# Optimization experiments

Measured on AMD Instinct MI355X. Metric: run time of the kernel, lower is better.

Reference implementation:

```python
import jax, jax.numpy as jnp
import numpy as np

B, T, E, H = 256, 128, 300, 2048


def setup_inputs() -> dict:
    key = jax.random.key(0)
    k0, k1, k2, k3, k4 = jax.random.split(key, 5)
    s = 1.0 / np.sqrt(H)  # PyTorch LSTM init range
    return {
        "x": jax.random.normal(k0, (B, T, E), dtype=jnp.float32),
        "W_ih": jax.random.uniform(k1, (4 * H, E), dtype=jnp.float32, minval=-s, maxval=s),
        "W_hh": jax.random.uniform(k2, (4 * H, H), dtype=jnp.float32, minval=-s, maxval=s),
        "b_ih": jax.random.uniform(k3, (4 * H,), dtype=jnp.float32, minval=-s, maxval=s),
        "b_hh": jax.random.uniform(k4, (4 * H,), dtype=jnp.float32, minval=-s, maxval=s),
    }


def reference(x, W_ih, W_hh, b_ih, b_hh):
    # x: [B, T, E]; returns final hidden state h_T: [B, H]
    Bn = x.shape[0]
    Hn = W_hh.shape[1]
    # Precompute input-to-gate projection for all timesteps: [B, T, 4H]
    x_gates = jnp.einsum('bte,ge->btg', x, W_ih) + b_ih + b_hh

    def step(carry, xg_t):
        h, c = carry
        gates = xg_t + h @ W_hh.T  # [B, 4H]
        i, f, g, o = jnp.split(gates, 4, axis=-1)  # PyTorch gate order i,f,g,o
        i = jax.nn.sigmoid(i)
        f = jax.nn.sigmoid(f)
        g = jnp.tanh(g)
        o = jax.nn.sigmoid(o)
        c = f * c + i * g
        h = o * jnp.tanh(c)
        return (h, c), None

    h0 = jnp.zeros((Bn, Hn), dtype=x.dtype)
    c0 = jnp.zeros((Bn, Hn), dtype=x.dtype)
    (h_T, _), _ = jax.lax.scan(step, (h0, c0), jnp.swapaxes(x_gates, 0, 1))
    return h_T
```

## Files before the change

### kernel.cpp

```cpp
#include <hip/hip_runtime.h>

typedef unsigned short u16;
typedef unsigned int u32;
typedef __bf16 bf16x8 __attribute__((ext_vector_type(8)));
typedef float f32x4 __attribute__((ext_vector_type(4)));

#define B_ 256
#define T_ 128
#define E_ 300
#define EP 320
#define H_ 2048
#define G_ 8192

#define OFF_XBF   0UL
#define OFF_WIH   20971520UL
#define OFF_WHH   26214400UL
#define OFF_BIAS  59768832UL
#define OFF_HBUF  59801600UL
#define OFF_BAR   61898752UL

#define GLDS16(gp, sp)                                                    \
  __builtin_amdgcn_global_load_lds(                                       \
      (__attribute__((address_space(1))) void*)(void*)(gp),               \
      (__attribute__((address_space(3))) void*)(sp), 16, 0, 0)
#define GLDS16C(gp, sp)                                                   \
  __builtin_amdgcn_global_load_lds(                                       \
      (__attribute__((address_space(1))) void*)(void*)(gp),               \
      (__attribute__((address_space(3))) void*)(sp), 16, 0, 17)

__device__ __forceinline__ u16 f2bf(float f) {
  u32 u = __builtin_bit_cast(u32, f);
  return (u16)((u + 0x7FFFu + ((u >> 16) & 1u)) >> 16);
}
__device__ __forceinline__ float sigm_f(float x) {
  return __builtin_amdgcn_rcpf(1.0f + __expf(-x));
}
__device__ __forceinline__ float tanh_f(float x) {
  return 1.0f - 2.0f * __builtin_amdgcn_rcpf(1.0f + __expf(2.0f * x));
}

__global__ void prep_kernel(const float* __restrict__ x, const float* __restrict__ Wih,
                            const float* __restrict__ Whh, const float* __restrict__ bih,
                            const float* __restrict__ bhh, u16* __restrict__ xbf,
                            u16* __restrict__ wihb, u16* __restrict__ whhb,
                            float* __restrict__ biasc, u32* __restrict__ bar) {
  const long NX = (long)T_ * B_ * EP;
  const long NWIH = (long)G_ * EP;
  const long NWHH = (long)G_ * H_;
  const long NBS = G_;
  const long NBAR = T_;
  const long total = NX + NWIH + NWHH + NBS + NBAR;
  for (long q = (long)blockIdx.x * blockDim.x + threadIdx.x; q < total;
       q += (long)gridDim.x * blockDim.x) {
    long r = q;
    if (r < NX) {
      int t = (int)(r / (B_ * EP));
      int rem = (int)(r % (B_ * EP));
      int b = rem / EP, e = rem % EP;
      float v = (e < E_) ? x[((long)b * T_ + t) * E_ + e] : 0.0f;
      xbf[r] = f2bf(v);
    } else if ((r -= NX) < NWIH) {
      int n = (int)(r / EP), e = (int)(r % EP);
      wihb[r] = f2bf((e < E_) ? Wih[(long)n * E_ + e] : 0.0f);
    } else if ((r -= NWIH) < NWHH) {
      whhb[r] = f2bf(Whh[r]);
    } else if ((r -= NWHH) < NBS) {
      biasc[r] = bih[r] + bhh[r];
    } else {
      r -= NBS;
      bar[r] = 0;
    }
  }
}

__global__ void __launch_bounds__(256, 1)
lstm_kernel(const u16* __restrict__ xbf, const u16* __restrict__ wihb,
            const u16* __restrict__ whhb, const float* __restrict__ biasc,
            u16* __restrict__ hbuf, u32* __restrict__ bar, float* __restrict__ out) {
  __shared__ __align__(16) u16 As[2][64 * 64];
  __shared__ __align__(16) u16 Bs[2][128 * 64];

  const int tid = threadIdx.x;
  const int l = tid & 63;
  const int w = tid >> 6;
  const int wr = w >> 1, wj = w & 1;
  const int bid = blockIdx.x;
  const int b0 = (bid >> 6) << 6;
  const int j0 = (bid & 63) << 5;
  const int jc = j0 + (wj << 4) + (l & 15);
  const int cgl = (tid & 7) ^ ((tid >> 3) & 7);

  const float bi = biasc[jc];
  const float bff = biasc[2048 + jc];
  const float bg = biasc[4096 + jc];
  const float bo = biasc[6144 + jc];

  float cst[2][4];
#pragma unroll
  for (int mi = 0; mi < 2; ++mi)
#pragma unroll
    for (int r = 0; r < 4; ++r) cst[mi][r] = 0.0f;

  auto stageA = [&](const u16* srcA, int strA, int kk, int p, bool coh) {
    u16* Ad = &As[p][w * 512];
#pragma unroll
    for (int i = 0; i < 2; ++i) {
      int slot = i * 256 + tid;
      const u16* g = srcA + (size_t)(slot >> 3) * strA + kk + cgl * 8;
      if (coh) { GLDS16C(g, Ad + i * 2048); } else { GLDS16(g, Ad + i * 2048); }
    }
  };
  auto stageB = [&](const u16* srcB, int strB, int kk, int p) {
    u16* Bd = &Bs[p][w * 512];
#pragma unroll
    for (int i = 0; i < 4; ++i) {
      int slot = i * 256 + tid;
      int nl = slot >> 3;
      int grow = ((nl >> 5) << 11) + j0 + (nl & 31);
      const u16* g = srcB + (size_t)grow * strB + kk + cgl * 8;
      GLDS16(g, Bd + i * 2048);
    }
  };

#pragma unroll 1
  for (int t = 0; t < T_; ++t) {
    const u16* hcur = hbuf + (size_t)(t & 1) * (B_ * H_) + (size_t)b0 * H_;
    u16* hnxt = hbuf + (size_t)((t + 1) & 1) * (B_ * H_);
    const u16* xsrc = xbf + (size_t)t * (B_ * EP) + (size_t)b0 * EP;

    f32x4 acc[2][4];
#pragma unroll
    for (int mi = 0; mi < 2; ++mi)
#pragma unroll
      for (int g = 0; g < 4; ++g) acc[mi][g] = (f32x4){0.f, 0.f, 0.f, 0.f};

    auto compute = [&](int p) {
#pragma unroll
      for (int k2 = 0; k2 < 2; ++k2) {
        int cp = ((k2 << 2) + (l >> 4)) ^ (l & 7);
        const u16* ap = &As[p][((wr << 5) + (l & 15)) * 64 + cp * 8];
        bf16x8 a0 = *(const bf16x8*)ap;
        bf16x8 a1 = *(const bf16x8*)(ap + 1024);
        const u16* bp = &Bs[p][((wj << 4) + (l & 15)) * 64 + cp * 8];
        bf16x8 bv0 = *(const bf16x8*)bp;
        bf16x8 bv1 = *(const bf16x8*)(bp + 2048);
        bf16x8 bv2 = *(const bf16x8*)(bp + 4096);
        bf16x8 bv3 = *(const bf16x8*)(bp + 6144);
        acc[0][0] = __builtin_amdgcn_mfma_f32_16x16x32_bf16(a0, bv0, acc[0][0], 0, 0, 0);
        acc[0][1] = __builtin_amdgcn_mfma_f32_16x16x32_bf16(a0, bv1, acc[0][1], 0, 0, 0);
        acc[0][2] = __builtin_amdgcn_mfma_f32_16x16x32_bf16(a0, bv2, acc[0][2], 0, 0, 0);
        acc[0][3] = __builtin_amdgcn_mfma_f32_16x16x32_bf16(a0, bv3, acc[0][3], 0, 0, 0);
        acc[1][0] = __builtin_amdgcn_mfma_f32_16x16x32_bf16(a1, bv0, acc[1][0], 0, 0, 0);
        acc[1][1] = __builtin_amdgcn_mfma_f32_16x16x32_bf16(a1, bv1, acc[1][1], 0, 0, 0);
        acc[1][2] = __builtin_amdgcn_mfma_f32_16x16x32_bf16(a1, bv2, acc[1][2], 0, 0, 0);
        acc[1][3] = __builtin_amdgcn_mfma_f32_16x16x32_bf16(a1, bv3, acc[1][3], 0, 0, 0);
      }
    };

    int p = 0;
    stageA(xsrc, EP, 0, 0, false);
    stageB(wihb, EP, 0, 0);
    __syncthreads();
#pragma unroll 1
    for (int kx = 0; kx < 5; ++kx) {
      if (kx < 4) {
        stageA(xsrc, EP, (kx + 1) << 6, p ^ 1, false);
        stageB(wihb, EP, (kx + 1) << 6, p ^ 1);
      }
      compute(p);
      __syncthreads();
      p ^= 1;
    }

    if (t > 0) {
      if (tid == 0) {
        while (__hip_atomic_load(&bar[t - 1], __ATOMIC_RELAXED,
                                 __HIP_MEMORY_SCOPE_AGENT) < 256u)
          __builtin_amdgcn_s_sleep(2);
      }
      __syncthreads();
      stageA(hcur, H_, 0, p, true);
      stageB(whhb, H_, 0, p);
      __syncthreads();
#pragma unroll 1
      for (int kh = 0; kh < 32; ++kh) {
        if (kh < 31) {
          stageA(hcur, H_, (kh + 1) << 6, p ^ 1, true);
          stageB(whhb, H_, (kh + 1) << 6, p ^ 1);
        }
        compute(p);
        __syncthreads();
        p ^= 1;
      }
    }

#pragma unroll
    for (int mi = 0; mi < 2; ++mi) {
#pragma unroll
      for (int r = 0; r < 4; ++r) {
        float ig = sigm_f(acc[mi][0][r] + bi);
        float fg = sigm_f(acc[mi][1][r] + bff);
        float gg = tanh_f(acc[mi][2][r] + bg);
        float og = sigm_f(acc[mi][3][r] + bo);
        float c = fg * cst[mi][r] + ig * gg;
        cst[mi][r] = c;
        float h = og * tanh_f(c);
        int row = b0 + (wr << 5) + (mi << 4) + ((l >> 4) << 2) + r;
        if (t < T_ - 1) {
          u16 hv = f2bf(h);
          u16* hp = hnxt + (size_t)row * H_ + jc;
          asm volatile("global_store_short %0, %1, off sc0 sc1"
                       :: "v"(hp), "v"((u32)hv) : "memory");
        } else {
          out[(size_t)row * H_ + jc] = h;
        }
      }
    }

    if (t < T_ - 1) {
      __builtin_amdgcn_s_waitcnt(0);
      __syncthreads();
      if (tid == 0)
        __hip_atomic_fetch_add(&bar[t], 1u, __ATOMIC_RELAXED,
                               __HIP_MEMORY_SCOPE_AGENT);
    }
  }
}

extern "C" void kernel_launch(void* const* d_in, const int* in_sizes, int n_in,
                              void* d_out, int out_size, void* d_ws, size_t ws_size,
                              hipStream_t stream) {
  const float* x = (const float*)d_in[0];
  const float* Wih = (const float*)d_in[1];
  const float* Whh = (const float*)d_in[2];
  const float* bih = (const float*)d_in[3];
  const float* bhh = (const float*)d_in[4];
  char* ws = (char*)d_ws;
  u16* xbf = (u16*)(ws + OFF_XBF);
  u16* wihb = (u16*)(ws + OFF_WIH);
  u16* whhb = (u16*)(ws + OFF_WHH);
  float* biasc = (float*)(ws + OFF_BIAS);
  u16* hbuf = (u16*)(ws + OFF_HBUF);
  u32* bar = (u32*)(ws + OFF_BAR);
  float* out = (float*)d_out;

  hipLaunchKernelGGL(prep_kernel, dim3(2048), dim3(256), 0, stream,
                     x, Wih, Whh, bih, bhh, xbf, wihb, whhb, biasc, bar);

  void* args[] = {(void*)&xbf, (void*)&wihb, (void*)&whhb,
                  (void*)&biasc, (void*)&hbuf, (void*)&bar, (void*)&out};
  hipLaunchCooperativeKernel((void*)lstm_kernel, dim3(256), dim3(256), args, 0, stream);
}
```

Baseline: 3.783 ms.

## Load GEMM operands directly into registers and give each timestep its own h buffer

Drops the LDS staging (global_load_lds with a swizzle, plus __syncthreads per k-step) and has each wave load its A and B fragments straight from global memory into registers, double-buffered in registers. The ping-pong h buffer becomes a per-timestep buffer, and the flag value read from the barrier (always below 2^31, so it adds 0) is folded into the h address so the compiler cannot hoist or cache the h loads ahead of the spin. This removes LDS round-trips and block-wide barriers, but each wave now issues redundant, less coalesced global loads for shared tiles. The h loads also lose the coherent cache-bypass flag.

After: 7.268 ms. 1.92x slower.

```diff
diff --git a/kernel.cpp b/kernel.cpp
--- a/kernel.cpp
+++ b/kernel.cpp
@@ -16,17 +16,8 @@
 #define OFF_WIH   20971520UL
 #define OFF_WHH   26214400UL
 #define OFF_BIAS  59768832UL
-#define OFF_HBUF  59801600UL
-#define OFF_BAR   61898752UL
-
-#define GLDS16(gp, sp)                                                    \
-  __builtin_amdgcn_global_load_lds(                                       \
-      (__attribute__((address_space(1))) void*)(void*)(gp),               \
-      (__attribute__((address_space(3))) void*)(sp), 16, 0, 0)
-#define GLDS16C(gp, sp)                                                   \
-  __builtin_amdgcn_global_load_lds(                                       \
-      (__attribute__((address_space(1))) void*)(void*)(gp),               \
-      (__attribute__((address_space(3))) void*)(sp), 16, 0, 17)
+#define OFF_BAR   59801600UL
+#define OFF_HBUF  59802112UL
 
 __device__ __forceinline__ u16 f2bf(float f) {
   u32 u = __builtin_bit_cast(u32, f);
@@ -76,10 +67,7 @@
 __global__ void __launch_bounds__(256, 1)
 lstm_kernel(const u16* __restrict__ xbf, const u16* __restrict__ wihb,
             const u16* __restrict__ whhb, const float* __restrict__ biasc,
-            u16* __restrict__ hbuf, u32* __restrict__ bar, float* __restrict__ out) {
-  __shared__ __align__(16) u16 As[2][64 * 64];
-  __shared__ __align__(16) u16 Bs[2][128 * 64];
-
+            u16* __restrict__ hbufs, u32* __restrict__ bar, float* __restrict__ out) {
   const int tid = threadIdx.x;
   const int l = tid & 63;
   const int w = tid >> 6;
@@ -87,8 +75,9 @@
   const int bid = blockIdx.x;
   const int b0 = (bid >> 6) << 6;
   const int j0 = (bid & 63) << 5;
+  const int arow = (wr << 5) + (l & 15);
+  const int koff = (l >> 4) << 3;
   const int jc = j0 + (wj << 4) + (l & 15);
-  const int cgl = (tid & 7) ^ ((tid >> 3) & 7);
 
   const float bi = biasc[jc];
   const float bff = biasc[2048 + jc];
@@ -101,99 +90,70 @@
 #pragma unroll
     for (int r = 0; r < 4; ++r) cst[mi][r] = 0.0f;
 
-  auto stageA = [&](const u16* srcA, int strA, int kk, int p, bool coh) {
-    u16* Ad = &As[p][w * 512];
-#pragma unroll
-    for (int i = 0; i < 2; ++i) {
-      int slot = i * 256 + tid;
-      const u16* g = srcA + (size_t)(slot >> 3) * strA + kk + cgl * 8;
-      if (coh) { GLDS16C(g, Ad + i * 2048); } else { GLDS16(g, Ad + i * 2048); }
-    }
-  };
-  auto stageB = [&](const u16* srcB, int strB, int kk, int p) {
-    u16* Bd = &Bs[p][w * 512];
-#pragma unroll
-    for (int i = 0; i < 4; ++i) {
-      int slot = i * 256 + tid;
-      int nl = slot >> 3;
-      int grow = ((nl >> 5) << 11) + j0 + (nl & 31);
-      const u16* g = srcB + (size_t)grow * strB + kk + cgl * 8;
-      GLDS16(g, Bd + i * 2048);
+  __shared__ u32 fv_sh;
+
+  f32x4 acc[2][4];
+
+  auto gemm_phase = [&](const u16* asrc, int astr, const u16* bsrc, int bstr,
+                        int kiters) {
+    bf16x8 af[2][2][2];
+    bf16x8 bfr[2][2][4];
+    auto ld = [&](int buf, int kk) {
+#pragma unroll
+      for (int mi = 0; mi < 2; ++mi)
+#pragma unroll
+        for (int k2 = 0; k2 < 2; ++k2)
+          af[buf][mi][k2] = *(const bf16x8*)(asrc +
+              (size_t)(arow + (mi << 4)) * astr + kk + (k2 << 5) + koff);
+#pragma unroll
+      for (int k2 = 0; k2 < 2; ++k2)
+#pragma unroll
+        for (int g = 0; g < 4; ++g)
+          bfr[buf][k2][g] = *(const bf16x8*)(bsrc +
+              (size_t)((g << 11) + jc) * bstr + kk + (k2 << 5) + koff);
+    };
+    ld(0, 0);
+#pragma unroll 2
+    for (int k = 0; k < kiters; ++k) {
+      int cur = k & 1;
+      if (k + 1 < kiters) ld(cur ^ 1, (k + 1) << 6);
+#pragma unroll
+      for (int k2 = 0; k2 < 2; ++k2)
+#pragma unroll
+        for (int g = 0; g < 4; ++g) {
+          acc[0][g] = __builtin_amdgcn_mfma_f32_16x16x32_bf16(
+              af[cur][0][k2], bfr[cur][k2][g], acc[0][g], 0, 0, 0);
+          acc[1][g] = __builtin_amdgcn_mfma_f32_16x16x32_bf16(
+              af[cur][1][k2], bfr[cur][k2][g], acc[1][g], 0, 0, 0);
+        }
     }
   };
 
 #pragma unroll 1
   for (int t = 0; t < T_; ++t) {
-    const u16* hcur = hbuf + (size_t)(t & 1) * (B_ * H_) + (size_t)b0 * H_;
-    u16* hnxt = hbuf + (size_t)((t + 1) & 1) * (B_ * H_);
+#pragma unroll
+    for (int mi = 0; mi < 2; ++mi)
+#pragma unroll
+      for (int g = 0; g < 4; ++g) acc[mi][g] = (f32x4){0.f, 0.f, 0.f, 0.f};
+
     const u16* xsrc = xbf + (size_t)t * (B_ * EP) + (size_t)b0 * EP;
-
-    f32x4 acc[2][4];
-#pragma unroll
-    for (int mi = 0; mi < 2; ++mi)
-#pragma unroll
-      for (int g = 0; g < 4; ++g) acc[mi][g] = (f32x4){0.f, 0.f, 0.f, 0.f};
-
-    auto compute = [&](int p) {
-#pragma unroll
-      for (int k2 = 0; k2 < 2; ++k2) {
-        int cp = ((k2 << 2) + (l >> 4)) ^ (l & 7);
-        const u16* ap = &As[p][((wr << 5) + (l & 15)) * 64 + cp * 8];
-        bf16x8 a0 = *(const bf16x8*)ap;
-        bf16x8 a1 = *(const bf16x8*)(ap + 1024);
-        const u16* bp = &Bs[p][((wj << 4) + (l & 15)) * 64 + cp * 8];
-        bf16x8 bv0 = *(const bf16x8*)bp;
-        bf16x8 bv1 = *(const bf16x8*)(bp + 2048);
-        bf16x8 bv2 = *(const bf16x8*)(bp + 4096);
-        bf16x8 bv3 = *(const bf16x8*)(bp + 6144);
-        acc[0][0] = __builtin_amdgcn_mfma_f32_16x16x32_bf16(a0, bv0, acc[0][0], 0, 0, 0);
-        acc[0][1] = __builtin_amdgcn_mfma_f32_16x16x32_bf16(a0, bv1, acc[0][1], 0, 0, 0);
-        acc[0][2] = __builtin_amdgcn_mfma_f32_16x16x32_bf16(a0, bv2, acc[0][2], 0, 0, 0);
-        acc[0][3] = __builtin_amdgcn_mfma_f32_16x16x32_bf16(a0, bv3, acc[0][3], 0, 0, 0);
-        acc[1][0] = __builtin_amdgcn_mfma_f32_16x16x32_bf16(a1, bv0, acc[1][0], 0, 0, 0);
-        acc[1][1] = __builtin_amdgcn_mfma_f32_16x16x32_bf16(a1, bv1, acc[1][1], 0, 0, 0);
-        acc[1][2] = __builtin_amdgcn_mfma_f32_16x16x32_bf16(a1, bv2, acc[1][2], 0, 0, 0);
-        acc[1][3] = __builtin_amdgcn_mfma_f32_16x16x32_bf16(a1, bv3, acc[1][3], 0, 0, 0);
-      }
-    };
-
-    int p = 0;
-    stageA(xsrc, EP, 0, 0, false);
-    stageB(wihb, EP, 0, 0);
-    __syncthreads();
-#pragma unroll 1
-    for (int kx = 0; kx < 5; ++kx) {
-      if (kx < 4) {
-        stageA(xsrc, EP, (kx + 1) << 6, p ^ 1, false);
-        stageB(wihb, EP, (kx + 1) << 6, p ^ 1);
-      }
-      compute(p);
-      __syncthreads();
-      p ^= 1;
-    }
+    gemm_phase(xsrc, EP, wihb, EP, 5);
 
     if (t > 0) {
       if (tid == 0) {
-        while (__hip_atomic_load(&bar[t - 1], __ATOMIC_RELAXED,
-                                 __HIP_MEMORY_SCOPE_AGENT) < 256u)
+        u32 f;
+        while ((f = __hip_atomic_load(&bar[t - 1], __ATOMIC_RELAXED,
+                                      __HIP_MEMORY_SCOPE_AGENT)) < 256u)
           __builtin_amdgcn_s_sleep(2);
+        fv_sh = f;
       }
       __syncthreads();
-      stageA(hcur, H_, 0, p, true);
-      stageB(whhb, H_, 0, p);
-      __syncthreads();
-#pragma unroll 1
-      for (int kh = 0; kh < 32; ++kh) {
-        if (kh < 31) {
-          stageA(hcur, H_, (kh + 1) << 6, p ^ 1, true);
-          stageB(whhb, H_, (kh + 1) << 6, p ^ 1);
-        }
-        compute(p);
-        __syncthreads();
-        p ^= 1;
-      }
-    }
-
+      const u16* hsrc = hbufs + (size_t)(t - 1) * (B_ * H_) +
+                        (size_t)b0 * H_ + (fv_sh >> 31);
+      gemm_phase(hsrc, H_, whhb, H_, 32);
+    }
+
+    u16* hnxt = hbufs + (size_t)t * (B_ * H_);
 #pragma unroll
     for (int mi = 0; mi < 2; ++mi) {
 #pragma unroll
@@ -240,14 +200,14 @@
   u16* wihb = (u16*)(ws + OFF_WIH);
   u16* whhb = (u16*)(ws + OFF_WHH);
   float* biasc = (float*)(ws + OFF_BIAS);
-  u16* hbuf = (u16*)(ws + OFF_HBUF);
   u32* bar = (u32*)(ws + OFF_BAR);
+  u16* hbufs = (u16*)(ws + OFF_HBUF);
   float* out = (float*)d_out;
 
   hipLaunchKernelGGL(prep_kernel, dim3(2048), dim3(256), 0, stream,
                      x, Wih, Whh, bih, bhh, xbf, wihb, whhb, biasc, bar);
 
   void* args[] = {(void*)&xbf, (void*)&wihb, (void*)&whhb,
-                  (void*)&biasc, (void*)&hbuf, (void*)&bar, (void*)&out};
+                  (void*)&biasc, (void*)&hbufs, (void*)&bar, (void*)&out};
   hipLaunchCooperativeKernel((void*)lstm_kernel, dim3(256), dim3(256), args, 0, stream);
 }
```

## Store each step's hidden state in its own buffer and drop coherent loads

Applied to the files above, without the earlier changes.

Each timestep now writes h to its own slice of a T-deep buffer instead of ping-ponging between two, so reads of h no longer need the sc0/sc1 coherent cache policy and use a nontemporal hint instead. Since no buffer is ever reused, stale cache lines cannot alias across steps. The flag value read from the barrier is folded into the address (always zero) to create a dependency. The cooperative launch is replaced by a normal launch. This trades a much larger workspace and reliance on fresh addresses for cheaper cached loads, and drops the co-residency guarantee for the spin barrier.

Result: slower. 4.853 ms (+28.3%).

```diff
diff --git a/kernel.cpp b/kernel.cpp
--- a/kernel.cpp
+++ b/kernel.cpp
@@ -16,17 +16,17 @@
 #define OFF_WIH   20971520UL
 #define OFF_WHH   26214400UL
 #define OFF_BIAS  59768832UL
-#define OFF_HBUF  59801600UL
-#define OFF_BAR   61898752UL
+#define OFF_BAR   59801600UL
+#define OFF_HBUF  59802112UL
 
 #define GLDS16(gp, sp)                                                    \
   __builtin_amdgcn_global_load_lds(                                       \
       (__attribute__((address_space(1))) void*)(void*)(gp),               \
       (__attribute__((address_space(3))) void*)(sp), 16, 0, 0)
-#define GLDS16C(gp, sp)                                                   \
+#define GLDS16NT(gp, sp)                                                  \
   __builtin_amdgcn_global_load_lds(                                       \
       (__attribute__((address_space(1))) void*)(void*)(gp),               \
-      (__attribute__((address_space(3))) void*)(sp), 16, 0, 17)
+      (__attribute__((address_space(3))) void*)(sp), 16, 0, 2)
 
 __device__ __forceinline__ u16 f2bf(float f) {
   u32 u = __builtin_bit_cast(u32, f);
@@ -76,9 +76,10 @@
 __global__ void __launch_bounds__(256, 1)
 lstm_kernel(const u16* __restrict__ xbf, const u16* __restrict__ wihb,
             const u16* __restrict__ whhb, const float* __restrict__ biasc,
-            u16* __restrict__ hbuf, u32* __restrict__ bar, float* __restrict__ out) {
+            u16* __restrict__ hbufs, u32* __restrict__ bar, float* __restrict__ out) {
   __shared__ __align__(16) u16 As[2][64 * 64];
   __shared__ __align__(16) u16 Bs[2][128 * 64];
+  __shared__ u32 fv_sh;
 
   const int tid = threadIdx.x;
   const int l = tid & 63;
@@ -87,8 +88,9 @@
   const int bid = blockIdx.x;
   const int b0 = (bid >> 6) << 6;
   const int j0 = (bid & 63) << 5;
-  const int jc = j0 + (wj << 4) + (l & 15);
-  const int cgl = (tid & 7) ^ ((tid >> 3) & 7);
+  const int v = l & 15;
+  const int q = l >> 4;
+  const int jc = j0 + (wj << 4) + v;
 
   const float bi = biasc[jc];
   const float bff = biasc[2048 + jc];
@@ -101,70 +103,68 @@
 #pragma unroll
     for (int r = 0; r < 4; ++r) cst[mi][r] = 0.0f;
 
-  auto stageA = [&](const u16* srcA, int strA, int kk, int p, bool coh) {
+  auto stageA = [&](const u16* src, int strA, int kk, int p) {
     u16* Ad = &As[p][w * 512];
 #pragma unroll
     for (int i = 0; i < 2; ++i) {
       int slot = i * 256 + tid;
-      const u16* g = srcA + (size_t)(slot >> 3) * strA + kk + cgl * 8;
-      if (coh) { GLDS16C(g, Ad + i * 2048); } else { GLDS16(g, Ad + i * 2048); }
+      int row = slot >> 3;
+      const u16* g = src + (size_t)row * strA + kk + (((tid & 7) ^ (row & 7)) << 3);
+      GLDS16NT(g, Ad + i * 2048);
     }
   };
-  auto stageB = [&](const u16* srcB, int strB, int kk, int p) {
+  auto stageB = [&](const u16* src, int strB, int kk, int p) {
     u16* Bd = &Bs[p][w * 512];
 #pragma unroll
     for (int i = 0; i < 4; ++i) {
       int slot = i * 256 + tid;
       int nl = slot >> 3;
       int grow = ((nl >> 5) << 11) + j0 + (nl & 31);
-      const u16* g = srcB + (size_t)grow * strB + kk + cgl * 8;
+      const u16* g = src + (size_t)grow * strB + kk + (((tid & 7) ^ (nl & 7)) << 3);
       GLDS16(g, Bd + i * 2048);
     }
   };
 
+  f32x4 acc[2][4];
+  auto compute = [&](int p) {
+#pragma unroll
+    for (int k2 = 0; k2 < 2; ++k2) {
+      int cs = ((k2 << 2) + q) ^ (l & 7);
+      const u16* ap = &As[p][((wr << 5) + v) * 64 + cs * 8];
+      bf16x8 a0 = *(const bf16x8*)ap;
+      bf16x8 a1 = *(const bf16x8*)(ap + 1024);
+      const u16* bp = &Bs[p][((wj << 4) + v) * 64 + cs * 8];
+      bf16x8 bv0 = *(const bf16x8*)bp;
+      bf16x8 bv1 = *(const bf16x8*)(bp + 2048);
+      bf16x8 bv2 = *(const bf16x8*)(bp + 4096);
+      bf16x8 bv3 = *(const bf16x8*)(bp + 6144);
+      acc[0][0] = __builtin_amdgcn_mfma_f32_16x16x32_bf16(a0, bv0, acc[0][0], 0, 0, 0);
+      acc[0][1] = __builtin_amdgcn_mfma_f32_16x16x32_bf16(a0, bv1, acc[0][1], 0, 0, 0);
+      acc[0][2] = __builtin_amdgcn_mfma_f32_16x16x32_bf16(a0, bv2, acc[0][2], 0, 0, 0);
+      acc[0][3] = __builtin_amdgcn_mfma_f32_16x16x32_bf16(a0, bv3, acc[0][3], 0, 0, 0);
+      acc[1][0] = __builtin_amdgcn_mfma_f32_16x16x32_bf16(a1, bv0, acc[1][0], 0, 0, 0);
+      acc[1][1] = __builtin_amdgcn_mfma_f32_16x16x32_bf16(a1, bv1, acc[1][1], 0, 0, 0);
+      acc[1][2] = __builtin_amdgcn_mfma_f32_16x16x32_bf16(a1, bv2, acc[1][2], 0, 0, 0);
+      acc[1][3] = __builtin_amdgcn_mfma_f32_16x16x32_bf16(a1, bv3, acc[1][3], 0, 0, 0);
+    }
+  };
+
+  int p = 0;
 #pragma unroll 1
   for (int t = 0; t < T_; ++t) {
-    const u16* hcur = hbuf + (size_t)(t & 1) * (B_ * H_) + (size_t)b0 * H_;
-    u16* hnxt = hbuf + (size_t)((t + 1) & 1) * (B_ * H_);
+#pragma unroll
+    for (int mi = 0; mi < 2; ++mi)
+#pragma unroll
+      for (int g = 0; g < 4; ++g) acc[mi][g] = (f32x4){0.f, 0.f, 0.f, 0.f};
+
     const u16* xsrc = xbf + (size_t)t * (B_ * EP) + (size_t)b0 * EP;
-
-    f32x4 acc[2][4];
-#pragma unroll
-    for (int mi = 0; mi < 2; ++mi)
-#pragma unroll
-      for (int g = 0; g < 4; ++g) acc[mi][g] = (f32x4){0.f, 0.f, 0.f, 0.f};
-
-    auto compute = [&](int p) {
-#pragma unroll
-      for (int k2 = 0; k2 < 2; ++k2) {
-        int cp = ((k2 << 2) + (l >> 4)) ^ (l & 7);
-        const u16* ap = &As[p][((wr << 5) + (l & 15)) * 64 + cp * 8];
-        bf16x8 a0 = *(const bf16x8*)ap;
-        bf16x8 a1 = *(const bf16x8*)(ap + 1024);
-        const u16* bp = &Bs[p][((wj << 4) + (l & 15)) * 64 + cp * 8];
-        bf16x8 bv0 = *(const bf16x8*)bp;
-        bf16x8 bv1 = *(const bf16x8*)(bp + 2048);
-        bf16x8 bv2 = *(const bf16x8*)(bp + 4096);
-        bf16x8 bv3 = *(const bf16x8*)(bp + 6144);
-        acc[0][0] = __builtin_amdgcn_mfma_f32_16x16x32_bf16(a0, bv0, acc[0][0], 0, 0, 0);
-        acc[0][1] = __builtin_amdgcn_mfma_f32_16x16x32_bf16(a0, bv1, acc[0][1], 0, 0, 0);
-        acc[0][2] = __builtin_amdgcn_mfma_f32_16x16x32_bf16(a0, bv2, acc[0][2], 0, 0, 0);
-        acc[0][3] = __builtin_amdgcn_mfma_f32_16x16x32_bf16(a0, bv3, acc[0][3], 0, 0, 0);
-        acc[1][0] = __builtin_amdgcn_mfma_f32_16x16x32_bf16(a1, bv0, acc[1][0], 0, 0, 0);
-        acc[1][1] = __builtin_amdgcn_mfma_f32_16x16x32_bf16(a1, bv1, acc[1][1], 0, 0, 0);
-        acc[1][2] = __builtin_amdgcn_mfma_f32_16x16x32_bf16(a1, bv2, acc[1][2], 0, 0, 0);
-        acc[1][3] = __builtin_amdgcn_mfma_f32_16x16x32_bf16(a1, bv3, acc[1][3], 0, 0, 0);
-      }
-    };
-
-    int p = 0;
-    stageA(xsrc, EP, 0, 0, false);
-    stageB(wihb, EP, 0, 0);
+    stageA(xsrc, EP, 0, p);
+    stageB(wihb, EP, 0, p);
     __syncthreads();
 #pragma unroll 1
     for (int kx = 0; kx < 5; ++kx) {
       if (kx < 4) {
-        stageA(xsrc, EP, (kx + 1) << 6, p ^ 1, false);
+        stageA(xsrc, EP, (kx + 1) << 6, p ^ 1);
         stageB(wihb, EP, (kx + 1) << 6, p ^ 1);
       }
       compute(p);
@@ -174,18 +174,22 @@
 
     if (t > 0) {
       if (tid == 0) {
-        while (__hip_atomic_load(&bar[t - 1], __ATOMIC_RELAXED,
-                                 __HIP_MEMORY_SCOPE_AGENT) < 256u)
+        u32 f;
+        while ((f = __hip_atomic_load(&bar[t - 1], __ATOMIC_RELAXED,
+                                      __HIP_MEMORY_SCOPE_AGENT)) < 256u)
           __builtin_amdgcn_s_sleep(2);
-      }
-      __syncthreads();
-      stageA(hcur, H_, 0, p, true);
+        fv_sh = f;
+      }
+      __syncthreads();
+      const u16* hsrc = hbufs + (size_t)(t - 1) * (B_ * H_) + (size_t)b0 * H_ +
+                        (fv_sh >> 31);
+      stageA(hsrc, H_, 0, p);
       stageB(whhb, H_, 0, p);
       __syncthreads();
 #pragma unroll 1
       for (int kh = 0; kh < 32; ++kh) {
         if (kh < 31) {
-          stageA(hcur, H_, (kh + 1) << 6, p ^ 1, true);
+          stageA(hsrc, H_, (kh + 1) << 6, p ^ 1);
           stageB(whhb, H_, (kh + 1) << 6, p ^ 1);
         }
         compute(p);
@@ -194,6 +198,7 @@
       }
     }
 
+    u16* hnxt = hbufs + (size_t)t * (B_ * H_);
 #pragma unroll
     for (int mi = 0; mi < 2; ++mi) {
 #pragma unroll
@@ -205,7 +210,7 @@
         float c = fg * cst[mi][r] + ig * gg;
         cst[mi][r] = c;
         float h = og * tanh_f(c);
-        int row = b0 + (wr << 5) + (mi << 4) + ((l >> 4) << 2) + r;
+        int row = b0 + (wr << 5) + (mi << 4) + (q << 2) + r;
         if (t < T_ - 1) {
           u16 hv = f2bf(h);
           u16* hp = hnxt + (size_t)row * H_ + jc;
@@ -240,14 +245,13 @@
   u16* wihb = (u16*)(ws + OFF_WIH);
   u16* whhb = (u16*)(ws + OFF_WHH);
   float* biasc = (float*)(ws + OFF_BIAS);
-  u16* hbuf = (u16*)(ws + OFF_HBUF);
   u32* bar = (u32*)(ws + OFF_BAR);
+  u16* hbufs = (u16*)(ws + OFF_HBUF);
   float* out = (float*)d_out;
 
   hipLaunchKernelGGL(prep_kernel, dim3(2048), dim3(256), 0, stream,
                      x, Wih, Whh, bih, bhh, xbf, wihb, whhb, biasc, bar);
 
-  void* args[] = {(void*)&xbf, (void*)&wihb, (void*)&whhb,
-                  (void*)&biasc, (void*)&hbuf, (void*)&bar, (void*)&out};
-  hipLaunchCooperativeKernel((void*)lstm_kernel, dim3(256), dim3(256), args, 0, stream);
-}
+  hipLaunchKernelGGL(lstm_kernel, dim3(256), dim3(256), 0, stream,
+                     xbf, wihb, whhb, biasc, hbufs, bar, out);
+}
```
